# Kernel optimization log

Measured on AMD Instinct MI355X. Metric: run time of the kernel, lower is better.

The kernel has to match this reference:

```python
import jax, jax.numpy as jnp
import numpy as np

C_IN = 1.0
C_OUT = 1.0
N_NODES = 10000
D_IN = 256
D_OUT = 256
N_EDGES = 320000
MIN_NORM = 1e-15
BALL_EPS = 4e-3  # float32 boundary eps used by HGCN PoincareBall


def _norm(x):
    return jnp.maximum(jnp.linalg.norm(x, axis=-1, keepdims=True), MIN_NORM)


def _artanh(x):
    x = jnp.clip(x, -1.0 + 1e-7, 1.0 - 1e-7)
    return 0.5 * (jnp.log1p(x) - jnp.log1p(-x))


def proj(x, c):
    norm = _norm(x)
    maxnorm = (1.0 - BALL_EPS) / jnp.sqrt(c)
    return jnp.where(norm > maxnorm, x / norm * maxnorm, x)


def expmap0(u, c):
    sc = jnp.sqrt(c)
    un = _norm(u)
    return jnp.tanh(sc * un) * u / (sc * un)


def logmap0(p, c):
    sc = jnp.sqrt(c)
    pn = _norm(p)
    return _artanh(sc * pn) * p / (sc * pn)


def mobius_add(x, y, c):
    x2 = jnp.sum(x * x, -1, keepdims=True)
    y2 = jnp.sum(y * y, -1, keepdims=True)
    xy = jnp.sum(x * y, -1, keepdims=True)
    num = (1 + 2 * c * xy + c * y2) * x + (1 - c * x2) * y
    denom = 1 + 2 * c * xy + c * c * x2 * y2
    return num / jnp.maximum(denom, MIN_NORM)


def mobius_matvec(m, x, c):
    sc = jnp.sqrt(c)
    xn = _norm(x)
    mx = x @ m.T  # [N, D_out]
    mxn = _norm(mx)
    res = jnp.tanh(mxn / xn * _artanh(sc * xn)) * mx / (mxn * sc)
    cond = jnp.all(mx == 0, axis=-1, keepdims=True)
    return jnp.where(cond, jnp.zeros_like(res), res)


def setup_inputs() -> dict:
    key = jax.random.key(0)
    k = jax.random.split(key, 6)
    x = jax.random.normal(k[0], (N_NODES, D_IN), jnp.float32) * 0.05
    x = proj(x, C_IN)  # valid points on the Poincare ball
    weight = jax.random.normal(k[1], (D_OUT, D_IN), jnp.float32) * (1.0 / np.sqrt(D_IN))
    bias = jax.random.normal(k[2], (D_OUT,), jnp.float32) * 0.01
    adj_val = jax.random.uniform(k[3], (N_EDGES,), jnp.float32) * (1.0 / 32.0)
    adj_row = jnp.sort(jax.random.randint(k[4], (N_EDGES,), 0, N_NODES, jnp.int32))
    adj_col = jax.random.randint(k[5], (N_EDGES,), 0, N_NODES, jnp.int32)
    return {"x": x, "weight": weight, "bias": bias, "adj_val": adj_val,
            "adj_row": adj_row, "adj_col": adj_col}


def reference(x, weight, bias, adj_val, adj_row, adj_col):
    # --- HypLinear: mobius matvec + hyperbolic bias ---
    h = proj(mobius_matvec(weight, x, C_IN), C_IN)
    hyp_bias = proj(expmap0(bias[None, :], C_IN), C_IN)  # proj_tan0 is identity
    h = proj(mobius_add(h, hyp_bias, C_IN), C_IN)
    # --- HypAgg: tangent-space sparse aggregation ---
    x_t = logmap0(h, C_IN)  # [N, D_out]
    msgs = adj_val[:, None] * x_t[adj_col]  # [E, D_out]
    support_t = jax.ops.segment_sum(msgs, adj_row, num_segments=N_NODES)
    h = proj(expmap0(support_t, C_IN), C_IN)
    # --- HypAct: act in tangent space, remap with c_out ---
    xt = jax.nn.relu(logmap0(h, C_IN))
    return proj(expmap0(xt, C_OUT), C_OUT)
```

## Files before the change

### kernel.cpp

```cpp
#include <hip/hip_runtime.h>
#include <math.h>

#define D 256
#define MAXNORM (1.0f - 4e-3f)
#define MIN_NORM 1e-15f

typedef _Float16 v8h __attribute__((ext_vector_type(8)));
typedef _Float16 h4  __attribute__((ext_vector_type(4)));
typedef float    v4f __attribute__((ext_vector_type(4)));

__device__ __forceinline__ float wave_reduce_sum(float v) {
    #pragma unroll
    for (int m = 32; m >= 1; m >>= 1) v += __shfl_xor(v, m, 64);
    return v;
}

__device__ __forceinline__ float dot4(const float4& a, const float4& b) {
    return a.x * b.x + a.y * b.y + a.z * b.z + a.w * b.w;
}

__device__ __forceinline__ float artanh_clip(float x) {
    x = fminf(fmaxf(x, -1.0f + 1e-7f), 1.0f - 1e-7f);
    return 0.5f * (log1pf(x) - log1pf(-x));
}

__global__ __launch_bounds__(256) void prep_kernel(
    const float* __restrict__ bias, const float* __restrict__ W,
    const int* __restrict__ rows,
    float* __restrict__ HB, _Float16* __restrict__ Wh,
    int* __restrict__ rowptr, int N, int E)
{
    const int b = blockIdx.x, t = threadIdx.x;
    const int e = b * 256 + t;

    if (e < E) {
        int r1 = rows[e];
        if (e == 0) {
            for (int r = 0; r <= r1; ++r) rowptr[r] = 0;
        } else {
            int r0 = rows[e - 1];
            for (int r = r0 + 1; r <= r1; ++r) rowptr[r] = e;
        }
        if (e == E - 1) {
            for (int r = r1 + 1; r <= N; ++r) rowptr[r] = E;
        }
    }

    if (b < 64) {
        int i = b * 256 + t;
        float4 v = ((const float4*)W)[i];
        h4 o; o[0] = (_Float16)v.x; o[1] = (_Float16)v.y;
        o[2] = (_Float16)v.z; o[3] = (_Float16)v.w;
        *(h4*)(Wh + 4 * (size_t)i) = o;
    }

    if (b == 64 && t < 64) {
        int l = t;
        float4 v = *(const float4*)(bias + 4 * l);
        float bn = fmaxf(sqrtf(wave_reduce_sum(dot4(v, v))), MIN_NORM);
        float f = tanhf(bn) / bn;
        float4 h = make_float4(v.x * f, v.y * f, v.z * f, v.w * f);
        float hn = fmaxf(sqrtf(wave_reduce_sum(dot4(h, h))), MIN_NORM);
        float s = (hn > MAXNORM) ? (MAXNORM / hn) : 1.0f;
        h.x *= s; h.y *= s; h.z *= s; h.w *= s;
        *(float4*)(HB + 4 * l) = h;
        float y2 = wave_reduce_sum(dot4(h, h));
        if (l == 0) HB[D] = y2;
    }
}

#define AS16 264

__global__ __launch_bounds__(256) void gemmrow_kernel(
    const float* __restrict__ X, const _Float16* __restrict__ Wh,
    const float* __restrict__ HB, unsigned char* __restrict__ XT8,
    float* __restrict__ SCg, int N)
{
    __shared__ _Float16 As[16 * AS16];
    __shared__ float xnsq[16];
    __shared__ float part_s[16][4];
    __shared__ float part_d[16][4];
    __shared__ float Arow[16], Brow[16];
    __shared__ float pmax[16][4];
    __shared__ float Srow[16];
    __shared__ unsigned char stage[16 * 256];

    const int t = threadIdx.x;
    const int r0 = blockIdx.x * 16;

    {
        const int r = t >> 4, q2 = t & 15;
        const int grow = r0 + r;
        float ss = 0.0f;
        #pragma unroll
        for (int j = 0; j < 4; ++j) {
            const int fi = q2 + j * 16;
            float4 v = make_float4(0.f, 0.f, 0.f, 0.f);
            if (grow < N) v = ((const float4*)X)[(size_t)grow * 64 + fi];
            ss += dot4(v, v);
            h4 hv; hv[0] = (_Float16)v.x; hv[1] = (_Float16)v.y;
            hv[2] = (_Float16)v.z; hv[3] = (_Float16)v.w;
            *(h4*)&As[r * AS16 + fi * 4] = hv;
        }
        ss += __shfl_xor(ss, 1, 64);
        ss += __shfl_xor(ss, 2, 64);
        ss += __shfl_xor(ss, 4, 64);
        ss += __shfl_xor(ss, 8, 64);
        if (q2 == 0) xnsq[r] = ss;
    }
    __syncthreads();

    const int w  = t >> 6;
    const int l  = t & 63;
    const int lm = l & 15;
    const int q  = l >> 4;

    v4f acc[4];
    #pragma unroll
    for (int ct = 0; ct < 4; ++ct)
        #pragma unroll
        for (int i = 0; i < 4; ++i) acc[ct][i] = 0.0f;

    const _Float16* WhB = Wh + (size_t)(64 * w + lm) * 256 + q * 8;

    #pragma unroll
    for (int kc = 0; kc < 8; ++kc) {
        v8h a = *(const v8h*)&As[lm * AS16 + kc * 32 + q * 8];
        #pragma unroll
        for (int ct = 0; ct < 4; ++ct) {
            v8h bfr = *(const v8h*)(WhB + (size_t)ct * 16 * 256 + kc * 32);
            acc[ct] = __builtin_amdgcn_mfma_f32_16x16x32_f16(a, bfr, acc[ct], 0, 0, 0);
        }
    }

    float yv[4];
    #pragma unroll
    for (int ct = 0; ct < 4; ++ct) yv[ct] = HB[64 * w + ct * 16 + lm];

    {
        float s_[4], d_[4];
        #pragma unroll
        for (int i = 0; i < 4; ++i) {
            float s = 0.f, d = 0.f;
            #pragma unroll
            for (int ct = 0; ct < 4; ++ct) {
                float v = acc[ct][i];
                s = fmaf(v, v, s);
                d = fmaf(v, yv[ct], d);
            }
            #pragma unroll
            for (int m = 1; m <= 8; m <<= 1) {
                s += __shfl_xor(s, m, 64);
                d += __shfl_xor(d, m, 64);
            }
            s_[i] = s; d_[i] = d;
        }
        if (lm == 0) {
            #pragma unroll
            for (int i = 0; i < 4; ++i) {
                part_s[q * 4 + i][w] = s_[i];
                part_d[q * 4 + i][w] = d_[i];
            }
        }
    }
    __syncthreads();

    if (t < 16) {
        float mx2 = part_s[t][0] + part_s[t][1] + part_s[t][2] + part_s[t][3];
        float mxy = part_d[t][0] + part_d[t][1] + part_d[t][2] + part_d[t][3];
        float y2  = HB[D];
        float xn  = fmaxf(sqrtf(xnsq[t]), MIN_NORM);
        float mxn = fmaxf(sqrtf(mx2), MIN_NORM);
        float r  = (mxn / xn) * artanh_clip(xn);
        float th = tanhf(r);
        float f  = th / mxn;
        float hn = fmaxf(th, MIN_NORM);
        float s  = (hn > MAXNORM) ? (MAXNORM / hn) : 1.0f;
        float fs = f * s;
        float x2 = th * th * s * s;
        float xy  = fs * mxy;
        float ch  = 1.0f + 2.0f * xy + y2;
        float cy  = 1.0f - x2;
        float inv = 1.0f / fmaxf(1.0f + 2.0f * xy + x2 * y2, MIN_NORM);
        float alpha = ch * fs * inv;
        float beta  = cy * inv;
        float gss = alpha * alpha * mx2 + 2.0f * alpha * beta * mxy + beta * beta * y2;
        float gn  = fmaxf(sqrtf(gss), MIN_NORM);
        float s2  = (gn > MAXNORM) ? (MAXNORM / gn) : 1.0f;
        float pn  = fmaxf(gn * s2, MIN_NORM);
        float lf  = artanh_clip(pn) / pn;
        Arow[t] = lf * s2 * alpha;
        Brow[t] = lf * s2 * beta;
    }
    __syncthreads();

    {
        float vmax[4];
        #pragma unroll
        for (int i = 0; i < 4; ++i) {
            const int rr = q * 4 + i;
            float A = Arow[rr], B = Brow[rr];
            float m = 0.f;
            #pragma unroll
            for (int ct = 0; ct < 4; ++ct)
                m = fmaxf(m, fabsf(fmaf(A, acc[ct][i], B * yv[ct])));
            #pragma unroll
            for (int mk = 1; mk <= 8; mk <<= 1)
                m = fmaxf(m, __shfl_xor(m, mk, 64));
            vmax[i] = m;
        }
        if (lm == 0) {
            #pragma unroll
            for (int i = 0; i < 4; ++i) pmax[q * 4 + i][w] = vmax[i];
        }
    }
    __syncthreads();
    if (t < 16) {
        float rm = fmaxf(fmaxf(pmax[t][0], pmax[t][1]),
                         fmaxf(pmax[t][2], pmax[t][3]));
        Srow[t] = 127.0f / fmaxf(rm, 1e-30f);
        if (r0 + t < N) SCg[r0 + t] = rm * (1.0f / 127.0f);
    }
    __syncthreads();

    #pragma unroll
    for (int i = 0; i < 4; ++i) {
        const int rr = q * 4 + i;
        float A = Arow[rr], B = Brow[rr], S = Srow[rr];
        #pragma unroll
        for (int ct = 0; ct < 4; ++ct) {
            float v = fmaf(A, acc[ct][i], B * yv[ct]) * S;
            v = fminf(fmaxf(v, -127.0f), 127.0f);
            int qi = (int)rintf(v) + 128;
            stage[rr * 256 + 64 * w + ct * 16 + lm] = (unsigned char)qi;
        }
    }
    __syncthreads();
    {
        const int rr2 = t >> 4, seg = t & 15;
        if (r0 + rr2 < N)
            *(uint4*)(XT8 + (size_t)(r0 + rr2) * 256 + seg * 16) =
                *(const uint4*)&stage[rr2 * 256 + seg * 16];
    }
}

__global__ __launch_bounds__(256) void agg_kernel(
    const int* __restrict__ rowptr, const int* __restrict__ cols,
    const float* __restrict__ vals, const float* __restrict__ SCg,
    const unsigned int* __restrict__ XT8u,
    float* __restrict__ OUT, int N)
{
    int node = (int)((blockIdx.x * (size_t)blockDim.x + threadIdx.x) >> 6);
    int l = threadIdx.x & 63;
    if (node >= N) return;

    int start = rowptr[node];
    int end   = rowptr[node + 1];

    float4 acc = make_float4(0.f, 0.f, 0.f, 0.f);
    float sw = 0.0f;

    for (int base = start; base < end; base += 64) {
        int idx = base + l;
        bool ok = idx < end;
        int   myc = ok ? cols[idx] : 0;
        float myv = ok ? vals[idx] * SCg[myc] : 0.0f;
        int cnt = min(64, end - base);
        int cnt16 = (cnt + 15) & ~15;

        for (int j = 0; j < cnt16; j += 16) {
            int   cc[16];
            float ww[16];
            #pragma unroll
            for (int u = 0; u < 16; ++u) {
                cc[u] = __shfl(myc, j + u, 64);
                ww[u] = __shfl(myv, j + u, 64);
            }
            unsigned int mw[16];
            #pragma unroll
            for (int u = 0; u < 16; ++u)
                mw[u] = XT8u[(size_t)cc[u] * 64 + l];
            #pragma unroll
            for (int u = 0; u < 16; ++u) {
                float f0 = (float)( mw[u]        & 0xffu);
                float f1 = (float)((mw[u] >> 8)  & 0xffu);
                float f2 = (float)((mw[u] >> 16) & 0xffu);
                float f3 = (float)( mw[u] >> 24);
                acc.x = fmaf(ww[u], f0, acc.x);
                acc.y = fmaf(ww[u], f1, acc.y);
                acc.z = fmaf(ww[u], f2, acc.z);
                acc.w = fmaf(ww[u], f3, acc.w);
                sw += ww[u];
            }
        }
    }

    float corr = 128.0f * sw;
    acc.x -= corr; acc.y -= corr; acc.z -= corr; acc.w -= corr;

    float un = fmaxf(sqrtf(wave_reduce_sum(dot4(acc, acc))), MIN_NORM);
    float f = tanhf(un) / un;
    float4 h = make_float4(acc.x * f, acc.y * f, acc.z * f, acc.w * f);
    float hn = fmaxf(sqrtf(wave_reduce_sum(dot4(h, h))), MIN_NORM);
    float s = (hn > MAXNORM) ? (MAXNORM / hn) : 1.0f;
    h.x *= s; h.y *= s; h.z *= s; h.w *= s;
    float pn = fmaxf(hn * s, MIN_NORM);
    float lf = artanh_clip(pn) / pn;
    float4 tt = make_float4(fmaxf(h.x * lf, 0.f), fmaxf(h.y * lf, 0.f),
                            fmaxf(h.z * lf, 0.f), fmaxf(h.w * lf, 0.f));
    float un2 = fmaxf(sqrtf(wave_reduce_sum(dot4(tt, tt))), MIN_NORM);
    float f2 = tanhf(un2) / un2;
    float4 o = make_float4(tt.x * f2, tt.y * f2, tt.z * f2, tt.w * f2);
    float on = fmaxf(sqrtf(wave_reduce_sum(dot4(o, o))), MIN_NORM);
    float s2 = (on > MAXNORM) ? (MAXNORM / on) : 1.0f;
    o.x *= s2; o.y *= s2; o.z *= s2; o.w *= s2;

    *(float4*)(OUT + (size_t)node * D + 4 * l) = o;
}

extern "C" void kernel_launch(void* const* d_in, const int* in_sizes, int n_in,
                              void* d_out, int out_size, void* d_ws, size_t ws_size,
                              hipStream_t stream) {
    const float* X    = (const float*)d_in[0];
    const float* W    = (const float*)d_in[1];
    const float* bias = (const float*)d_in[2];
    const float* vals = (const float*)d_in[3];
    const int*   rows = (const int*)d_in[4];
    const int*   cols = (const int*)d_in[5];
    float* OUT = (float*)d_out;

    const int N = in_sizes[0] / D;
    const int E = in_sizes[3];

    int*           rowptr = (int*)d_ws;
    float*         HB  = (float*)d_ws + 10240;
    _Float16*      Wh  = (_Float16*)((float*)d_ws + 10240 + 512);
    float*         SCg = (float*)d_ws + 10240 + 512 + 32768;
    unsigned char* XT8 = (unsigned char*)((float*)d_ws + 10240 + 512 + 32768 + 10240);

    prep_kernel<<<(E + 255) / 256, 256, 0, stream>>>(bias, W, rows, HB, Wh, rowptr, N, E);
    gemmrow_kernel<<<(N + 15) / 16, 256, 0, stream>>>(X, Wh, HB, XT8, SCg, N);
    int wave_blocks = (N + 3) / 4;
    agg_kernel<<<wave_blocks, 256, 0, stream>>>(rowptr, cols, vals, SCg,
                                                (const unsigned int*)XT8, OUT, N);
}
```

Before: 108.3 us.

## Pre-swizzle fp16 weights into MFMA fragment order and double GEMM row tile

```diff
diff --git a/kernel.cpp b/kernel.cpp
--- a/kernel.cpp
+++ b/kernel.cpp
@@ -46,12 +46,24 @@
         }
     }
 
-    if (b < 64) {
-        int i = b * 256 + t;
-        float4 v = ((const float4*)W)[i];
-        h4 o; o[0] = (_Float16)v.x; o[1] = (_Float16)v.y;
-        o[2] = (_Float16)v.z; o[3] = (_Float16)v.w;
-        *(h4*)(Wh + 4 * (size_t)i) = o;
+    if (b < 32) {
+        int j  = b * 256 + t;
+        int l  = j & 63;
+        int g  = j >> 6;
+        int kc = g & 7;
+        int ct = (g >> 3) & 3;
+        int wc = g >> 5;
+        int col = wc * 64 + ct * 16 + (l & 15);
+        int kb  = kc * 32 + ((l >> 4) & 3) * 8;
+        const float* src = W + (size_t)col * 256 + kb;
+        float4 v0 = *(const float4*)src;
+        float4 v1 = *(const float4*)(src + 4);
+        v8h o;
+        o[0] = (_Float16)v0.x; o[1] = (_Float16)v0.y;
+        o[2] = (_Float16)v0.z; o[3] = (_Float16)v0.w;
+        o[4] = (_Float16)v1.x; o[5] = (_Float16)v1.y;
+        o[6] = (_Float16)v1.z; o[7] = (_Float16)v1.w;
+        *(v8h*)(Wh + (size_t)j * 8) = o;
     }
 
     if (b == 64 && t < 64) {
@@ -71,22 +83,22 @@
 
 #define AS16 264
 
-__global__ __launch_bounds__(256) void gemmrow_kernel(
+__global__ __launch_bounds__(512) void gemmrow_kernel(
     const float* __restrict__ X, const _Float16* __restrict__ Wh,
     const float* __restrict__ HB, unsigned char* __restrict__ XT8,
     float* __restrict__ SCg, int N)
 {
-    __shared__ _Float16 As[16 * AS16];
-    __shared__ float xnsq[16];
-    __shared__ float part_s[16][4];
-    __shared__ float part_d[16][4];
-    __shared__ float Arow[16], Brow[16];
-    __shared__ float pmax[16][4];
-    __shared__ float Srow[16];
-    __shared__ unsigned char stage[16 * 256];
+    __shared__ _Float16 As[32 * AS16];
+    __shared__ float xnsq[32];
+    __shared__ float part_s[32][4];
+    __shared__ float part_d[32][4];
+    __shared__ float Arow[32], Brow[32];
+    __shared__ float pmax[32][4];
+    __shared__ float Srow[32];
+    __shared__ unsigned char stage[32 * 256];
 
     const int t = threadIdx.x;
-    const int r0 = blockIdx.x * 16;
+    const int r0 = blockIdx.x * 32;
 
     {
         const int r = t >> 4, q2 = t & 15;
@@ -110,7 +122,9 @@
     }
     __syncthreads();
 
-    const int w  = t >> 6;
+    const int wv = t >> 6;
+    const int rh = wv >> 2;
+    const int wc = wv & 3;
     const int l  = t & 63;
     const int lm = l & 15;
     const int q  = l >> 4;
@@ -121,21 +135,20 @@
         #pragma unroll
         for (int i = 0; i < 4; ++i) acc[ct][i] = 0.0f;
 
-    const _Float16* WhB = Wh + (size_t)(64 * w + lm) * 256 + q * 8;
-
     #pragma unroll
     for (int kc = 0; kc < 8; ++kc) {
-        v8h a = *(const v8h*)&As[lm * AS16 + kc * 32 + q * 8];
+        v8h a = *(const v8h*)&As[(rh * 16 + lm) * AS16 + kc * 32 + q * 8];
         #pragma unroll
         for (int ct = 0; ct < 4; ++ct) {
-            v8h bfr = *(const v8h*)(WhB + (size_t)ct * 16 * 256 + kc * 32);
+            v8h bfr = *(const v8h*)(Wh +
+                (((size_t)(wc * 32 + ct * 8 + kc) * 64 + l) * 8));
             acc[ct] = __builtin_amdgcn_mfma_f32_16x16x32_f16(a, bfr, acc[ct], 0, 0, 0);
         }
     }
 
     float yv[4];
     #pragma unroll
-    for (int ct = 0; ct < 4; ++ct) yv[ct] = HB[64 * w + ct * 16 + lm];
+    for (int ct = 0; ct < 4; ++ct) yv[ct] = HB[64 * wc + ct * 16 + lm];
 
     {
         float s_[4], d_[4];
@@ -158,14 +171,14 @@
         if (lm == 0) {
             #pragma unroll
             for (int i = 0; i < 4; ++i) {
-                part_s[q * 4 + i][w] = s_[i];
-                part_d[q * 4 + i][w] = d_[i];
-            }
-        }
-    }
-    __syncthreads();
-
-    if (t < 16) {
+                part_s[rh * 16 + q * 4 + i][wc] = s_[i];
+                part_d[rh * 16 + q * 4 + i][wc] = d_[i];
+            }
+        }
+    }
+    __syncthreads();
+
+    if (t < 32) {
         float mx2 = part_s[t][0] + part_s[t][1] + part_s[t][2] + part_s[t][3];
         float mxy = part_d[t][0] + part_d[t][1] + part_d[t][2] + part_d[t][3];
         float y2  = HB[D];
@@ -198,7 +211,7 @@
         float vmax[4];
         #pragma unroll
         for (int i = 0; i < 4; ++i) {
-            const int rr = q * 4 + i;
+            const int rr = rh * 16 + q * 4 + i;
             float A = Arow[rr], B = Brow[rr];
             float m = 0.f;
             #pragma unroll
@@ -211,11 +224,11 @@
         }
         if (lm == 0) {
             #pragma unroll
-            for (int i = 0; i < 4; ++i) pmax[q * 4 + i][w] = vmax[i];
-        }
-    }
-    __syncthreads();
-    if (t < 16) {
+            for (int i = 0; i < 4; ++i) pmax[rh * 16 + q * 4 + i][wc] = vmax[i];
+        }
+    }
+    __syncthreads();
+    if (t < 32) {
         float rm = fmaxf(fmaxf(pmax[t][0], pmax[t][1]),
                          fmaxf(pmax[t][2], pmax[t][3]));
         Srow[t] = 127.0f / fmaxf(rm, 1e-30f);
@@ -225,14 +238,14 @@
 
     #pragma unroll
     for (int i = 0; i < 4; ++i) {
-        const int rr = q * 4 + i;
+        const int rr = rh * 16 + q * 4 + i;
         float A = Arow[rr], B = Brow[rr], S = Srow[rr];
         #pragma unroll
         for (int ct = 0; ct < 4; ++ct) {
             float v = fmaf(A, acc[ct][i], B * yv[ct]) * S;
             v = fminf(fmaxf(v, -127.0f), 127.0f);
             int qi = (int)rintf(v) + 128;
-            stage[rr * 256 + 64 * w + ct * 16 + lm] = (unsigned char)qi;
+            stage[rr * 256 + 64 * wc + ct * 16 + lm] = (unsigned char)qi;
         }
     }
     __syncthreads();
@@ -299,21 +312,20 @@
     acc.x -= corr; acc.y -= corr; acc.z -= corr; acc.w -= corr;
 
     float un = fmaxf(sqrtf(wave_reduce_sum(dot4(acc, acc))), MIN_NORM);
-    float f = tanhf(un) / un;
-    float4 h = make_float4(acc.x * f, acc.y * f, acc.z * f, acc.w * f);
-    float hn = fmaxf(sqrtf(wave_reduce_sum(dot4(h, h))), MIN_NORM);
-    float s = (hn > MAXNORM) ? (MAXNORM / hn) : 1.0f;
-    h.x *= s; h.y *= s; h.z *= s; h.w *= s;
+    float f  = tanhf(un) / un;
+    float hn = f * un;
+    float s  = (hn > MAXNORM) ? (MAXNORM / hn) : 1.0f;
     float pn = fmaxf(hn * s, MIN_NORM);
     float lf = artanh_clip(pn) / pn;
-    float4 tt = make_float4(fmaxf(h.x * lf, 0.f), fmaxf(h.y * lf, 0.f),
-                            fmaxf(h.z * lf, 0.f), fmaxf(h.w * lf, 0.f));
+    float g  = f * s * lf;
+    float4 tt = make_float4(fmaxf(acc.x * g, 0.f), fmaxf(acc.y * g, 0.f),
+                            fmaxf(acc.z * g, 0.f), fmaxf(acc.w * g, 0.f));
     float un2 = fmaxf(sqrtf(wave_reduce_sum(dot4(tt, tt))), MIN_NORM);
-    float f2 = tanhf(un2) / un2;
-    float4 o = make_float4(tt.x * f2, tt.y * f2, tt.z * f2, tt.w * f2);
-    float on = fmaxf(sqrtf(wave_reduce_sum(dot4(o, o))), MIN_NORM);
-    float s2 = (on > MAXNORM) ? (MAXNORM / on) : 1.0f;
-    o.x *= s2; o.y *= s2; o.z *= s2; o.w *= s2;
+    float f2  = tanhf(un2) / un2;
+    float on  = f2 * un2;
+    float s2  = (on > MAXNORM) ? (MAXNORM / on) : 1.0f;
+    float fo  = f2 * s2;
+    float4 o = make_float4(tt.x * fo, tt.y * fo, tt.z * fo, tt.w * fo);
 
     *(float4*)(OUT + (size_t)node * D + 4 * l) = o;
 }
@@ -339,7 +351,7 @@
     unsigned char* XT8 = (unsigned char*)((float*)d_ws + 10240 + 512 + 32768 + 10240);
 
     prep_kernel<<<(E + 255) / 256, 256, 0, stream>>>(bias, W, rows, HB, Wh, rowptr, N, E);
-    gemmrow_kernel<<<(N + 15) / 16, 256, 0, stream>>>(X, Wh, HB, XT8, SCg, N);
+    gemmrow_kernel<<<(N + 31) / 32, 512, 0, stream>>>(X, Wh, HB, XT8, SCg, N);
     int wave_blocks = (N + 3) / 4;
     agg_kernel<<<wave_blocks, 256, 0, stream>>>(rowptr, cols, vals, SCg,
                                                 (const unsigned int*)XT8, OUT, N);
```

After: 101.4 us. -6.4%, faster.
